# Kernel tuning notes

Hardware: AMD Instinct MI355X
Metric: run time of the kernel (lower is better)

The kernel has to match this reference:

```python
import jax, jax.numpy as jnp
import numpy as np

B, S, E, FF, Q = 8, 2048, 768, 3072, 8  # batch, seq, embed_dim, ffn_dim, n_qubits


def setup_inputs() -> dict:
    key = jax.random.key(0)
    k_x, k_phi, k_w1, k_w2 = jax.random.split(key, 4)
    x = jax.random.normal(k_x, (B, S, E), dtype=jnp.float32)
    # trainable RY angles (one per qubit), like tq.RY(has_params=True)
    phi = jax.random.normal(k_phi, (Q,), dtype=jnp.float32)
    # linear1: n_qubits -> ffn_dim ; linear2: ffn_dim -> embed_dim (torch layout [out, in])
    w1 = jax.random.normal(k_w1, (FF, Q), dtype=jnp.float32) / np.sqrt(Q).astype(np.float32)
    b1 = jnp.zeros((FF,), dtype=jnp.float32)
    w2 = jax.random.normal(k_w2, (E, FF), dtype=jnp.float32) / np.sqrt(FF).astype(np.float32)
    b2 = jnp.zeros((E,), dtype=jnp.float32)
    return {"x": x, "phi": phi, "w1": w1, "b1": b1, "w2": w2, "b2": b2}


def reference(x, phi, w1, b1, w2, b2):
    # Quantum block (exact closed form): for each token, encoder applies
    # RY(x_i) on wire i, then a trainable RY(phi_i) on wire i. Starting from
    # |0>^Q this is a product state; RY compose additively and
    # <Z> after RY(theta)|0> == cos(theta). MeasureAll(PauliZ) therefore gives:
    n_qubits = phi.shape[0]
    meas = jnp.cos(x[..., :n_qubits] + phi)          # [B, S, Q]
    # dropout is identity in eval mode
    h = jax.nn.relu(jnp.einsum('bsq,fq->bsf', meas, w1) + b1)  # [B, S, FF]
    return jnp.einsum('bsf,ef->bse', h, w2) + b2               # [B, S, E]
```

## Files before the change

### kernel.cpp

```cpp
#include <hip/hip_runtime.h>
#include <hip/hip_bf16.h>
#include <stdint.h>

#define M_TOK 16384
#define E_DIM 768
#define FF_DIM 3072
#define Q_N 8

typedef __attribute__((ext_vector_type(8))) short bf16x8;
typedef __attribute__((ext_vector_type(4))) float f32x4;

__device__ inline unsigned short f2bf(float f) {
  union { float f; unsigned u; } v; v.f = f;
  unsigned r = v.u + 0x7fffu + ((v.u >> 16) & 1u);
  return (unsigned short)(r >> 16);
}

__global__ __launch_bounds__(256) void cvt_w2(const float* __restrict__ w2,
                                              __hip_bfloat16* __restrict__ w2b) {
  int i = (blockIdx.x * 256 + threadIdx.x) * 4;
  const int n = E_DIM * FF_DIM;
  if (i < n) {
    float4 v = *(const float4*)(w2 + i);
    ushort4 o;
    o.x = f2bf(v.x); o.y = f2bf(v.y); o.z = f2bf(v.z); o.w = f2bf(v.w);
    *(ushort4*)((unsigned short*)w2b + i) = o;
  }
}

__global__ __launch_bounds__(256) void compute_h(const float* __restrict__ x,
                                                 const float* __restrict__ phi,
                                                 const float* __restrict__ w1,
                                                 const float* __restrict__ b1,
                                                 __hip_bfloat16* __restrict__ hout) {
  __shared__ float s_meas[32][8];
  const int t = threadIdx.x;
  const int bm = blockIdx.x / 6;
  const int bf = blockIdx.x % 6;
  const int m0 = bm * 32;
  const int f0 = bf * 512;

  if (t < 64) {
    int m = t >> 1, hh = t & 1;
    float4 v = *(const float4*)(x + (size_t)(m0 + m) * E_DIM + hh * 4);
    float4 p = *(const float4*)(phi + hh * 4);
    s_meas[m][hh * 4 + 0] = __cosf(v.x + p.x);
    s_meas[m][hh * 4 + 1] = __cosf(v.y + p.y);
    s_meas[m][hh * 4 + 2] = __cosf(v.z + p.z);
    s_meas[m][hh * 4 + 3] = __cosf(v.w + p.w);
  }
  __syncthreads();

  const float4* wr = (const float4*)(w1 + (size_t)(f0 + 2 * t) * Q_N);
  float4 a0 = wr[0], a1 = wr[1], b0 = wr[2], b1v = wr[3];
  float wA[8] = {a0.x, a0.y, a0.z, a0.w, a1.x, a1.y, a1.z, a1.w};
  float wB[8] = {b0.x, b0.y, b0.z, b0.w, b1v.x, b1v.y, b1v.z, b1v.w};
  const float biasA = b1[f0 + 2 * t];
  const float biasB = b1[f0 + 2 * t + 1];

  uint32_t* dst32 = (uint32_t*)hout;
  for (int m = 0; m < 32; ++m) {
    float a = biasA, b = biasB;
#pragma unroll
    for (int q = 0; q < 8; ++q) {
      float mv = s_meas[m][q];
      a = fmaf(mv, wA[q], a);
      b = fmaf(mv, wB[q], b);
    }
    a = fmaxf(a, 0.f);
    b = fmaxf(b, 0.f);
    uint32_t pack = (uint32_t)f2bf(a) | ((uint32_t)f2bf(b) << 16);
    dst32[(size_t)(m0 + m) * (FF_DIM / 2) + (f0 / 2) + t] = pack;
  }
}

#define GLDS16(g, l)                                                          \
  __builtin_amdgcn_global_load_lds(                                           \
      (const __attribute__((address_space(1))) void*)(g),                     \
      (__attribute__((address_space(3))) void*)(l), 16, 0, 0)

#define BUF_ELEMS 28672
#define B_OFF 16384

__global__ __launch_bounds__(512, 1) void gemm_bt(const __hip_bfloat16* __restrict__ A,
                                                  const __hip_bfloat16* __restrict__ Bw,
                                                  const float* __restrict__ b2,
                                                  float* __restrict__ C) {
  const int K = FF_DIM;
  const int N = E_DIM;

  __shared__ __align__(16) __hip_bfloat16 lds[2 * BUF_ELEMS];

  const int t = threadIdx.x;
  const int swz = (blockIdx.x & 7) * 32 + (blockIdx.x >> 3);
  const int bm = swz >> 2;
  const int bn = swz & 3;
  const size_t m0 = (size_t)bm * 256;
  const int n0 = bn * 192;

  const int w = t >> 6, l = t & 63;
  const int wr = w >> 2;
  const int wc = w & 3;
  const int lr = l & 15;
  const int lk = l >> 4;

  const int x0 = lk ^ (lr & 7);
  const int x1 = x0 ^ 4;
  const int baseA = (wr * 128 + lr) * 64;
  const int baseB = B_OFF + (wc * 48 + lr) * 64;
  const int offA0 = baseA + x0 * 8, offA1 = baseA + x1 * 8;
  const int offB0 = baseB + x0 * 8, offB1 = baseB + x1 * 8;

  const int rs = t >> 3;
  const int lc = (t & 7) ^ (rs & 7);
  const __hip_bfloat16* sA[4];
  const __hip_bfloat16* sB[3];
#pragma unroll
  for (int s = 0; s < 4; ++s) sA[s] = A + (m0 + s * 64 + rs) * (size_t)K + lc * 8;
#pragma unroll
  for (int s = 0; s < 3; ++s) sB[s] = Bw + ((size_t)n0 + s * 64 + rs) * K + lc * 8;

  f32x4 acc[8][3] = {};

#define STAGE(K0S, WBUF)                                                      \
  {                                                                           \
    __hip_bfloat16* ld = lds + (WBUF) * BUF_ELEMS + t * 8;                    \
    GLDS16(sA[0] + (K0S), ld);                                                \
    GLDS16(sA[1] + (K0S), ld + 4096);                                         \
    GLDS16(sA[2] + (K0S), ld + 8192);                                         \
    GLDS16(sA[3] + (K0S), ld + 12288);                                        \
    GLDS16(sB[0] + (K0S), ld + 16384);                                        \
    GLDS16(sB[1] + (K0S), ld + 20480);                                        \
    GLDS16(sB[2] + (K0S), ld + 24576);                                        \
  }

#define TILE(KT, RBUF, DO_STAGE)                                              \
  {                                                                           \
    if (DO_STAGE) STAGE(((KT) + 1) * 64, (RBUF) ^ 1);                         \
    const __hip_bfloat16* la = lds + (RBUF) * BUF_ELEMS;                      \
    bf16x8 af0[8], bfx0[3], af1[8], bfx1[3];                                  \
            \
    _Pragma("unroll") for (int mi = 0; mi < 8; ++mi)                          \
        af0[mi] = *(const bf16x8*)(la + offA0 + mi * 1024);                   \
    _Pragma("unroll") for (int ni = 0; ni < 3; ++ni)                          \
        bfx0[ni] = *(const bf16x8*)(la + offB0 + ni * 1024);                  \
    _Pragma("unroll") for (int mi = 0; mi < 8; ++mi)                          \
        af1[mi] = *(const bf16x8*)(la + offA1 + mi * 1024);                   \
    _Pragma("unroll") for (int ni = 0; ni < 3; ++ni)                          \
        bfx1[ni] = *(const bf16x8*)(la + offB1 + ni * 1024);                  \
    __builtin_amdgcn_s_setprio(1);                                            \
    _Pragma("unroll") for (int mi = 0; mi < 8; ++mi)                          \
        _Pragma("unroll") for (int ni = 0; ni < 3; ++ni)                      \
            acc[mi][ni] = __builtin_amdgcn_mfma_f32_16x16x32_bf16(            \
                af0[mi], bfx0[ni], acc[mi][ni], 0, 0, 0);                     \
    _Pragma("unroll") for (int mi = 0; mi < 8; ++mi)                          \
        _Pragma("unroll") for (int ni = 0; ni < 3; ++ni)                      \
            acc[mi][ni] = __builtin_amdgcn_mfma_f32_16x16x32_bf16(            \
                af1[mi], bfx1[ni], acc[mi][ni], 0, 0, 0);                     \
    __builtin_amdgcn_s_setprio(0);                                            \
    asm volatile("s_waitcnt vmcnt(0)" ::: "memory");                          \
    __builtin_amdgcn_s_barrier();                                             \
  }

  STAGE(0, 0);
  asm volatile("s_waitcnt vmcnt(0)" ::: "memory");
  __builtin_amdgcn_s_barrier();

#pragma unroll 1
  for (int tt = 0; tt < 46; tt += 2) {
    TILE(tt + 0, 0, 1);
    TILE(tt + 1, 1, 1);
  }
  TILE(46, 0, 1);
  TILE(47, 1, 0);

#undef TILE
#undef STAGE

#pragma unroll
  for (int mi = 0; mi < 8; ++mi) {
    const size_t row = m0 + wr * 128 + mi * 16 + lk * 4;
#pragma unroll
    for (int ni = 0; ni < 3; ++ni) {
      const int col = n0 + wc * 48 + ni * 16 + lr;
      const float bias = b2[col];
#pragma unroll
      for (int rr = 0; rr < 4; ++rr) {
        C[(row + rr) * N + col] = acc[mi][ni][rr] + bias;
      }
    }
  }
}

__global__ __launch_bounds__(256) void fallback_fused(const float* __restrict__ x,
                                                      const float* __restrict__ phi,
                                                      const float* __restrict__ w1,
                                                      const float* __restrict__ b1,
                                                      const float* __restrict__ w2,
                                                      const float* __restrict__ b2,
                                                      float* __restrict__ out) {
  __shared__ float s_h[FF_DIM];
  __shared__ float s_meas[Q_N];
  const int t = threadIdx.x;
  const size_t m = blockIdx.x;
  if (t < Q_N) s_meas[t] = __cosf(x[m * E_DIM + t] + phi[t]);
  __syncthreads();
  for (int f = t; f < FF_DIM; f += 256) {
    const float4* wr = (const float4*)(w1 + (size_t)f * Q_N);
    float4 a = wr[0], b = wr[1];
    float acc = b1[f];
    acc = fmaf(s_meas[0], a.x, acc); acc = fmaf(s_meas[1], a.y, acc);
    acc = fmaf(s_meas[2], a.z, acc); acc = fmaf(s_meas[3], a.w, acc);
    acc = fmaf(s_meas[4], b.x, acc); acc = fmaf(s_meas[5], b.y, acc);
    acc = fmaf(s_meas[6], b.z, acc); acc = fmaf(s_meas[7], b.w, acc);
    s_h[f] = fmaxf(acc, 0.f);
  }
  __syncthreads();
  for (int e = t; e < E_DIM; e += 256) {
    const float* w2r = w2 + (size_t)e * FF_DIM;
    float acc = b2[e];
    for (int f = 0; f < FF_DIM; f += 4) {
      float4 wv = *(const float4*)(w2r + f);
      acc = fmaf(s_h[f + 0], wv.x, acc);
      acc = fmaf(s_h[f + 1], wv.y, acc);
      acc = fmaf(s_h[f + 2], wv.z, acc);
      acc = fmaf(s_h[f + 3], wv.w, acc);
    }
    out[m * E_DIM + e] = acc;
  }
}

extern "C" void kernel_launch(void* const* d_in, const int* in_sizes, int n_in,
                              void* d_out, int out_size, void* d_ws, size_t ws_size,
                              hipStream_t stream) {
  const float* x   = (const float*)d_in[0];
  const float* phi = (const float*)d_in[1];
  const float* w1  = (const float*)d_in[2];
  const float* b1  = (const float*)d_in[3];
  const float* w2  = (const float*)d_in[4];
  const float* b2  = (const float*)d_in[5];
  float* out = (float*)d_out;

  const size_t H_BYTES   = (size_t)M_TOK * FF_DIM * 2;
  const size_t W2B_BYTES = (size_t)E_DIM * FF_DIM * 2;
  const size_t NEED = H_BYTES + W2B_BYTES;

  if (ws_size >= NEED) {
    __hip_bfloat16* h   = (__hip_bfloat16*)d_ws;
    __hip_bfloat16* w2b = (__hip_bfloat16*)((char*)d_ws + H_BYTES);
    cvt_w2<<<(E_DIM * FF_DIM) / (256 * 4), 256, 0, stream>>>(w2, w2b);
    compute_h<<<(M_TOK / 32) * (FF_DIM / 512), 256, 0, stream>>>(x, phi, w1, b1, h);
    gemm_bt<<<(M_TOK / 256) * (E_DIM / 192), 512, 0, stream>>>(h, w2b, b2, out);
  } else {
    fallback_fused<<<M_TOK, 256, 0, stream>>>(x, phi, w1, b1, w2, b2, out);
  }
}
```

Measured before the change: 98.88 us.

## Split GEMM k-tile into four barrier-synchronized phases interleaving LDS reads, prefetch, MFMA

Restructures each 64-wide k-tile of the second GEMM into four sub-phases. Each phase loads half the A fragments from LDS, issues part of the next tile's global-to-LDS prefetch, then runs a block of MFMAs at raised priority between workgroup barriers. The aim is a ping-pong style schedule that overlaps memory traffic with matrix work across waves and cuts register pressure from holding all fragments at once. It adds three extra barriers per tile, which can cost time if waves stall on each other.

```diff
diff --git a/kernel.cpp b/kernel.cpp
--- a/kernel.cpp
+++ b/kernel.cpp
@@ -122,47 +122,84 @@
 
   f32x4 acc[8][3] = {};
 
-#define STAGE(K0S, WBUF)                                                      \
+#define STAGE_A(K0S, WBUF)                                                    \
   {                                                                           \
     __hip_bfloat16* ld = lds + (WBUF) * BUF_ELEMS + t * 8;                    \
     GLDS16(sA[0] + (K0S), ld);                                                \
     GLDS16(sA[1] + (K0S), ld + 4096);                                         \
     GLDS16(sA[2] + (K0S), ld + 8192);                                         \
     GLDS16(sA[3] + (K0S), ld + 12288);                                        \
+  }
+#define STAGE_B(K0S, WBUF)                                                    \
+  {                                                                           \
+    __hip_bfloat16* ld = lds + (WBUF) * BUF_ELEMS + t * 8;                    \
     GLDS16(sB[0] + (K0S), ld + 16384);                                        \
     GLDS16(sB[1] + (K0S), ld + 20480);                                        \
     GLDS16(sB[2] + (K0S), ld + 24576);                                        \
   }
 
+#define PHASE_SYNC_IN()                                                       \
+  __builtin_amdgcn_s_barrier();                                               \
+  asm volatile("s_waitcnt lgkmcnt(0)" ::: "memory");                          \
+  __builtin_amdgcn_sched_barrier(0);                                          \
+  __builtin_amdgcn_s_setprio(1)
+
+#define PHASE_SYNC_OUT()                                                      \
+  __builtin_amdgcn_s_setprio(0);                                              \
+  __builtin_amdgcn_s_barrier()
+
 #define TILE(KT, RBUF, DO_STAGE)                                              \
   {                                                                           \
-    if (DO_STAGE) STAGE(((KT) + 1) * 64, (RBUF) ^ 1);                         \
     const __hip_bfloat16* la = lds + (RBUF) * BUF_ELEMS;                      \
-    bf16x8 af0[8], bfx0[3], af1[8], bfx1[3];                                  \
-            \
-    _Pragma("unroll") for (int mi = 0; mi < 8; ++mi)                          \
-        af0[mi] = *(const bf16x8*)(la + offA0 + mi * 1024);                   \
+    bf16x8 fa[4], fb0[3], fb1[3];                                             \
+          \
+    _Pragma("unroll") for (int mi = 0; mi < 4; ++mi)                          \
+        fa[mi] = *(const bf16x8*)(la + offA0 + mi * 1024);                    \
     _Pragma("unroll") for (int ni = 0; ni < 3; ++ni)                          \
-        bfx0[ni] = *(const bf16x8*)(la + offB0 + ni * 1024);                  \
-    _Pragma("unroll") for (int mi = 0; mi < 8; ++mi)                          \
-        af1[mi] = *(const bf16x8*)(la + offA1 + mi * 1024);                   \
+        fb0[ni] = *(const bf16x8*)(la + offB0 + ni * 1024);                   \
+    if (DO_STAGE) STAGE_A(((KT) + 1) * 64, (RBUF) ^ 1);                       \
+    PHASE_SYNC_IN();                                                          \
+    _Pragma("unroll") for (int mi = 0; mi < 4; ++mi)                          \
+      _Pragma("unroll") for (int ni = 0; ni < 3; ++ni)                        \
+        acc[mi][ni] = __builtin_amdgcn_mfma_f32_16x16x32_bf16(                \
+            fa[mi], fb0[ni], acc[mi][ni], 0, 0, 0);                           \
+    PHASE_SYNC_OUT();                                                         \
+          \
+    _Pragma("unroll") for (int mi = 0; mi < 4; ++mi)                          \
+        fa[mi] = *(const bf16x8*)(la + offA0 + (mi + 4) * 1024);              \
+    if (DO_STAGE) STAGE_B(((KT) + 1) * 64, (RBUF) ^ 1);                       \
+    PHASE_SYNC_IN();                                                          \
+    _Pragma("unroll") for (int mi = 0; mi < 4; ++mi)                          \
+      _Pragma("unroll") for (int ni = 0; ni < 3; ++ni)                        \
+        acc[mi + 4][ni] = __builtin_amdgcn_mfma_f32_16x16x32_bf16(            \
+            fa[mi], fb0[ni], acc[mi + 4][ni], 0, 0, 0);                       \
+    PHASE_SYNC_OUT();                                                         \
+                        \
+    _Pragma("unroll") for (int mi = 0; mi < 4; ++mi)                          \
+        fa[mi] = *(const bf16x8*)(la + offA1 + mi * 1024);                    \
     _Pragma("unroll") for (int ni = 0; ni < 3; ++ni)                          \
-        bfx1[ni] = *(const bf16x8*)(la + offB1 + ni * 1024);                  \
-    __builtin_amdgcn_s_setprio(1);                                            \
-    _Pragma("unroll") for (int mi = 0; mi < 8; ++mi)                          \
-        _Pragma("unroll") for (int ni = 0; ni < 3; ++ni)                      \
-            acc[mi][ni] = __builtin_amdgcn_mfma_f32_16x16x32_bf16(            \
-                af0[mi], bfx0[ni], acc[mi][ni], 0, 0, 0);                     \
-    _Pragma("unroll") for (int mi = 0; mi < 8; ++mi)                          \
-        _Pragma("unroll") for (int ni = 0; ni < 3; ++ni)                      \
-            acc[mi][ni] = __builtin_amdgcn_mfma_f32_16x16x32_bf16(            \
-                af1[mi], bfx1[ni], acc[mi][ni], 0, 0, 0);                     \
+        fb1[ni] = *(const bf16x8*)(la + offB1 + ni * 1024);                   \
+    PHASE_SYNC_IN();                                                          \
+    _Pragma("unroll") for (int mi = 0; mi < 4; ++mi)                          \
+      _Pragma("unroll") for (int ni = 0; ni < 3; ++ni)                        \
+        acc[mi][ni] = __builtin_amdgcn_mfma_f32_16x16x32_bf16(                \
+            fa[mi], fb1[ni], acc[mi][ni], 0, 0, 0);                           \
+    PHASE_SYNC_OUT();                                                         \
+       \
+    _Pragma("unroll") for (int mi = 0; mi < 4; ++mi)                          \
+        fa[mi] = *(const bf16x8*)(la + offA1 + (mi + 4) * 1024);              \
+    PHASE_SYNC_IN();                                                          \
+    _Pragma("unroll") for (int mi = 0; mi < 4; ++mi)                          \
+      _Pragma("unroll") for (int ni = 0; ni < 3; ++ni)                        \
+        acc[mi + 4][ni] = __builtin_amdgcn_mfma_f32_16x16x32_bf16(            \
+            fa[mi], fb1[ni], acc[mi + 4][ni], 0, 0, 0);                       \
     __builtin_amdgcn_s_setprio(0);                                            \
     asm volatile("s_waitcnt vmcnt(0)" ::: "memory");                          \
     __builtin_amdgcn_s_barrier();                                             \
   }
 
-  STAGE(0, 0);
+  STAGE_A(0, 0);
+  STAGE_B(0, 0);
   asm volatile("s_waitcnt vmcnt(0)" ::: "memory");
   __builtin_amdgcn_s_barrier();
 
@@ -175,7 +212,10 @@
   TILE(47, 1, 0);
 
 #undef TILE
-#undef STAGE
+#undef PHASE_SYNC_IN
+#undef PHASE_SYNC_OUT
+#undef STAGE_A
+#undef STAGE_B
 
 #pragma unroll
   for (int mi = 0; mi < 8; ++mi) {
```

After: 101.5 us. +2.6%, slower.

## Split K-tile prefetch into early and late halves with partial vmcnt waits

Applied to the files above, without the earlier changes.

Each 64-wide K step of the bf16 GEMM now runs in two halves of the M fragments. The prefetch of the next tile is split too: the B tile and the A rows needed first are issued early, and the other A rows are issued after the mid-tile barrier. Waits use partial vmcnt counts instead of draining all loads, so global-to-LDS copies can stay in flight across MFMA phases, and fewer A fragments are live in registers at once. The cost is an extra barrier per tile and a fragile dependence on the exact order and count of outstanding loads.

```diff
diff --git a/kernel.cpp b/kernel.cpp
--- a/kernel.cpp
+++ b/kernel.cpp
@@ -122,48 +122,76 @@
 
   f32x4 acc[8][3] = {};
 
-#define STAGE(K0S, WBUF)                                                      \
+#define S_EARLY(K0S, WBUF)                                                    \
   {                                                                           \
     __hip_bfloat16* ld = lds + (WBUF) * BUF_ELEMS + t * 8;                    \
-    GLDS16(sA[0] + (K0S), ld);                                                \
-    GLDS16(sA[1] + (K0S), ld + 4096);                                         \
-    GLDS16(sA[2] + (K0S), ld + 8192);                                         \
-    GLDS16(sA[3] + (K0S), ld + 12288);                                        \
     GLDS16(sB[0] + (K0S), ld + 16384);                                        \
     GLDS16(sB[1] + (K0S), ld + 20480);                                        \
     GLDS16(sB[2] + (K0S), ld + 24576);                                        \
+    GLDS16(sA[0] + (K0S), ld);                                                \
+    GLDS16(sA[2] + (K0S), ld + 8192);                                         \
+  }
+#define S_LATE(K0S, WBUF)                                                     \
+  {                                                                           \
+    __hip_bfloat16* ld = lds + (WBUF) * BUF_ELEMS + t * 8;                    \
+    GLDS16(sA[1] + (K0S), ld + 4096);                                         \
+    GLDS16(sA[3] + (K0S), ld + 12288);                                        \
   }
 
 #define TILE(KT, RBUF, DO_STAGE)                                              \
   {                                                                           \
-    if (DO_STAGE) STAGE(((KT) + 1) * 64, (RBUF) ^ 1);                         \
     const __hip_bfloat16* la = lds + (RBUF) * BUF_ELEMS;                      \
-    bf16x8 af0[8], bfx0[3], af1[8], bfx1[3];                                  \
-            \
-    _Pragma("unroll") for (int mi = 0; mi < 8; ++mi)                          \
-        af0[mi] = *(const bf16x8*)(la + offA0 + mi * 1024);                   \
-    _Pragma("unroll") for (int ni = 0; ni < 3; ++ni)                          \
-        bfx0[ni] = *(const bf16x8*)(la + offB0 + ni * 1024);                  \
-    _Pragma("unroll") for (int mi = 0; mi < 8; ++mi)                          \
-        af1[mi] = *(const bf16x8*)(la + offA1 + mi * 1024);                   \
-    _Pragma("unroll") for (int ni = 0; ni < 3; ++ni)                          \
-        bfx1[ni] = *(const bf16x8*)(la + offB1 + ni * 1024);                  \
+    if (DO_STAGE) S_EARLY(((KT) + 1) * 64, (RBUF) ^ 1);                       \
+    bf16x8 af0[4], af1[4], bfx0[3], bfx1[3];                                  \
+    _Pragma("unroll") for (int mi = 0; mi < 4; ++mi) {                        \
+      af0[mi] = *(const bf16x8*)(la + offA0 + mi * 1024);                     \
+      af1[mi] = *(const bf16x8*)(la + offA1 + mi * 1024);                     \
+    }                                                                         \
+    _Pragma("unroll") for (int ni = 0; ni < 3; ++ni) {                        \
+      bfx0[ni] = *(const bf16x8*)(la + offB0 + ni * 1024);                    \
+      bfx1[ni] = *(const bf16x8*)(la + offB1 + ni * 1024);                    \
+    }                                                                         \
     __builtin_amdgcn_s_setprio(1);                                            \
-    _Pragma("unroll") for (int mi = 0; mi < 8; ++mi)                          \
-        _Pragma("unroll") for (int ni = 0; ni < 3; ++ni)                      \
-            acc[mi][ni] = __builtin_amdgcn_mfma_f32_16x16x32_bf16(            \
-                af0[mi], bfx0[ni], acc[mi][ni], 0, 0, 0);                     \
-    _Pragma("unroll") for (int mi = 0; mi < 8; ++mi)                          \
-        _Pragma("unroll") for (int ni = 0; ni < 3; ++ni)                      \
-            acc[mi][ni] = __builtin_amdgcn_mfma_f32_16x16x32_bf16(            \
-                af1[mi], bfx1[ni], acc[mi][ni], 0, 0, 0);                     \
+    _Pragma("unroll") for (int mi = 0; mi < 4; ++mi)                          \
+      _Pragma("unroll") for (int ni = 0; ni < 3; ++ni)                        \
+        acc[mi][ni] = __builtin_amdgcn_mfma_f32_16x16x32_bf16(                \
+            af0[mi], bfx0[ni], acc[mi][ni], 0, 0, 0);                         \
+    _Pragma("unroll") for (int mi = 0; mi < 4; ++mi)                          \
+      _Pragma("unroll") for (int ni = 0; ni < 3; ++ni)                        \
+        acc[mi][ni] = __builtin_amdgcn_mfma_f32_16x16x32_bf16(                \
+            af1[mi], bfx1[ni], acc[mi][ni], 0, 0, 0);                         \
     __builtin_amdgcn_s_setprio(0);                                            \
-    asm volatile("s_waitcnt vmcnt(0)" ::: "memory");                          \
+    if (DO_STAGE) {                                                           \
+      asm volatile("s_waitcnt vmcnt(5)" ::: "memory");   \
+    } else {                                                                  \
+      asm volatile("s_waitcnt vmcnt(0)" ::: "memory");                        \
+    }                                                                         \
     __builtin_amdgcn_s_barrier();                                             \
-  }
-
-  STAGE(0, 0);
-  asm volatile("s_waitcnt vmcnt(0)" ::: "memory");
+    bf16x8 ag0[4], ag1[4];                                                    \
+    _Pragma("unroll") for (int mi = 0; mi < 4; ++mi) {                        \
+      ag0[mi] = *(const bf16x8*)(la + offA0 + (mi + 4) * 1024);               \
+      ag1[mi] = *(const bf16x8*)(la + offA1 + (mi + 4) * 1024);               \
+    }                                                                         \
+    if (DO_STAGE) S_LATE(((KT) + 1) * 64, (RBUF) ^ 1);                        \
+    __builtin_amdgcn_s_setprio(1);                                            \
+    _Pragma("unroll") for (int mi = 0; mi < 4; ++mi)                          \
+      _Pragma("unroll") for (int ni = 0; ni < 3; ++ni)                        \
+        acc[mi + 4][ni] = __builtin_amdgcn_mfma_f32_16x16x32_bf16(            \
+            ag0[mi], bfx0[ni], acc[mi + 4][ni], 0, 0, 0);                     \
+    _Pragma("unroll") for (int mi = 0; mi < 4; ++mi)                          \
+      _Pragma("unroll") for (int ni = 0; ni < 3; ++ni)                        \
+        acc[mi + 4][ni] = __builtin_amdgcn_mfma_f32_16x16x32_bf16(            \
+            ag1[mi], bfx1[ni], acc[mi + 4][ni], 0, 0, 0);                     \
+    __builtin_amdgcn_s_setprio(0);                                            \
+    if (DO_STAGE) {                                                           \
+      asm volatile("s_waitcnt vmcnt(2)" ::: "memory");  \
+      __builtin_amdgcn_s_barrier();                                           \
+    }                                                                         \
+  }
+
+  S_EARLY(0, 0);
+  S_LATE(0, 0);
+  asm volatile("s_waitcnt vmcnt(2)" ::: "memory");
   __builtin_amdgcn_s_barrier();
 
 #pragma unroll 1
@@ -175,7 +203,8 @@
   TILE(47, 1, 0);
 
 #undef TILE
-#undef STAGE
+#undef S_EARLY
+#undef S_LATE
 
 #pragma unroll
   for (int mi = 0; mi < 8; ++mi) {
```

After: 99.91 us. About the same (+1.0%).
